# Kernel tuning notes

Hardware: AMD Instinct MI355X
Metric: run time of the kernel (lower is better)

Reference implementation:

```python
import jax, jax.numpy as jnp
import numpy as np
from jax import lax

DN = ('NCHW', 'OIHW', 'NCHW')  # torch conv layout
QMIN, QMAX = -128.0, 127.0     # qint8 range


def setup_inputs() -> dict:
    key = jax.random.key(0)
    k1, k2, k3, k4 = jax.random.split(key, 4)
    B, Cin, Cout, H, W, K = 8, 320, 320, 64, 64, 3
    x = jax.random.normal(k1, (B, Cin, H, W), dtype=jnp.float32)
    # int8 weight values stored as int32 (int_repr of per-channel quantized weight)
    weight_int = jax.random.randint(k2, (Cout, Cin, K, K), -128, 128, dtype=jnp.int32)
    weight_scales = jax.random.uniform(k3, (Cout,), jnp.float32, 0.001, 0.01)
    act_scales = jnp.float32(0.04)        # per-tensor activation scale
    act_zero_points = jnp.float32(3.0)    # per-tensor activation zero point
    act_scales_inv = 1.0 / act_scales
    bias = jax.random.normal(k4, (Cout,), dtype=jnp.float32) * 0.1
    # precomputed buffers (from_float): padding>0 path
    weight_sum_by_input_channels = weight_int.astype(jnp.float32).sum(axis=1, keepdims=True)  # [O,1,K,K]
    scale = weight_scales * act_scales  # fused dequant scale per output channel
    return {
        'x': x,
        'weight_int': weight_int,
        'weight_sum_by_input_channels': weight_sum_by_input_channels,
        'scale': scale,
        'act_scales_inv': act_scales_inv,
        'act_zero_points': act_zero_points,
        'bias': bias,
    }


def reference(x, weight_int, weight_sum_by_input_channels, scale,
              act_scales_inv, act_zero_points, bias):
    stride, pad = 1, 1
    # per-tensor activation quantization: x_int = clamp(round(x/s) + zp)
    x_int = jnp.clip(jnp.round(x * act_scales_inv) + act_zero_points, QMIN, QMAX)
    w = weight_int.astype(jnp.float32)
    # integer conv (emulated in f32): conv(x_int, W_int)
    acc = lax.conv_general_dilated(x_int, w, (stride, stride),
                                   [(pad, pad), (pad, pad)], dimension_numbers=DN)
    # zero-point correction: zp * conv(ones, sum_i W_int) (spatially varying near padding)
    ones = jnp.ones_like(x[:, :1])  # [B,1,H,W]
    corr = lax.conv_general_dilated(ones, weight_sum_by_input_channels, (stride, stride),
                                    [(pad, pad), (pad, pad)], dimension_numbers=DN)
    corr = corr * act_zero_points
    # dequant: per-output-channel scale = w_scale * a_scale, plus float bias
    out = scale[None, :, None, None] * (acc - corr) + bias[None, :, None, None]
    return out
```

## Files before the change

### kernel.cpp

```cpp
#include <hip/hip_runtime.h>
#include <hip/hip_bf16.h>


typedef int v4i __attribute__((ext_vector_type(4)));

typedef const unsigned int __attribute__((address_space(1)))* gas_uptr;
typedef unsigned int __attribute__((address_space(3)))* las_uptr;

#define B_   8
#define CIN  320
#define COUT 320
#define H_   64
#define W_   64
#define HW_  4096
#define HP   66
#define WP   66
#define XPAD_BYTES (B_*HP*WP*CIN)
#define W8_BYTES (COUT*9*CIN)

__global__ __launch_bounds__(256) void repack_bias_kernel(const int* __restrict__ wint,
                                                          unsigned char* __restrict__ w8,
                                                          const float* __restrict__ wsum,
                                                          const float* __restrict__ scale,
                                                          const float* __restrict__ bias,
                                                          const float* __restrict__ zp_p,
                                                          float* __restrict__ be) {
    int j = blockIdx.x * 256 + threadIdx.x;
    if (j < COUT) {
        float s = 0.f;
        #pragma unroll
        for (int tp = 0; tp < 9; ++tp) s += wsum[j*9 + tp];
        be[j] = bias[j] - scale[j] * zp_p[0] * s;
    }
    int co  = j / 720;
    int r   = j - co * 720;
    int tap = r / 80;
    int d   = r - tap * 80;
    int ci  = d * 4;
    const int* base = wint + (co * CIN + ci) * 9 + tap;
    unsigned b0 = (unsigned)(base[0]  & 0xFF);
    unsigned b1 = (unsigned)(base[9]  & 0xFF);
    unsigned b2 = (unsigned)(base[18] & 0xFF);
    unsigned b3 = (unsigned)(base[27] & 0xFF);
    ((unsigned*)w8)[j] = b0 | (b1 << 8) | (b2 << 16) | (b3 << 24);
}

__global__ __launch_bounds__(256) void quant_pad_kernel(const float* __restrict__ x,
                                                        unsigned char* __restrict__ xpad,
                                                        const float* __restrict__ inv_p,
                                                        const float* __restrict__ zp_p) {
    __shared__ __align__(16) unsigned lds[64 * 81];
    int bid = blockIdx.x;
    int b  = bid / HP;
    int ph = bid - b * HP;
    int t  = threadIdx.x;
    float inv = inv_p[0];
    float zp  = zp_p[0];
    int zpi = (int)rintf(zp);
    unsigned zd = ((unsigned)(zpi & 0xFF)) * 0x01010101u;

    unsigned* rowbase = (unsigned*)(xpad + (size_t)((b * HP + ph) * WP) * CIN);

    if (ph == 0 || ph == HP - 1) {
        for (int j = t; j < WP * CIN / 4; j += 256) rowbase[j] = zd;
        return;
    }
    int h = ph - 1;
    const float* xrow = x + (size_t)b * CIN * H_ * W_ + h * W_;
    int wq = t & 15;
    int cg = t >> 4;
    #pragma unroll
    for (int i = 0; i < 5; ++i) {
        int ci0 = i * 64 + cg * 4;
        float4 f[4];
        #pragma unroll
        for (int jj = 0; jj < 4; ++jj)
            f[jj] = *(const float4*)(xrow + (size_t)(ci0 + jj) * HW_ + wq * 4);
        #pragma unroll
        for (int k = 0; k < 4; ++k) {
            unsigned d = 0;
            #pragma unroll
            for (int jj = 0; jj < 4; ++jj) {
                float v = (&f[jj].x)[k];
                float q = rintf(v * inv) + zp;
                q = fminf(fmaxf(q, -128.0f), 127.0f);
                int qi = (int)q;
                d |= ((unsigned)(qi & 0xFF)) << (8 * jj);
            }
            lds[(wq * 4 + k) * 81 + (ci0 >> 2)] = d;
        }
    }
    __syncthreads();
    if (t < 80)            rowbase[t] = zd;
    else if (t < 160)      rowbase[65 * 80 + (t - 80)] = zd;
    for (int j = t; j < 64 * 80; j += 256) {
        int p = j / 80;
        int d = j - p * 80;
        rowbase[80 + j] = lds[p * 81 + d];
    }
}

#define CHUNK_SLOTS 1056
#define ROUNDS 5
#define BUF_BYTES (ROUNDS * 256 * 16)

__global__ __launch_bounds__(256, 2) void conv_gemm_kernel(const unsigned char* __restrict__ xpad,
                                                           const unsigned char* __restrict__ w8,
                                                           const float* __restrict__ scale,
                                                           const float* __restrict__ be,
                                                           float* __restrict__ out) {
    __shared__ __align__(16) unsigned char Al[2 * BUF_BYTES];

    int t    = threadIdx.x;
    int lane = t & 63;
    int wave = t >> 6;
    int wm   = wave & 1;
    int wn   = wave >> 1;
    int m0   = blockIdx.x * 128;
    int n0   = blockIdx.y * 160;
    int b0   = m0 >> 12;
    int h0   = (m0 & 4095) >> 6;

    int srcoff[ROUNDS];
    #pragma unroll
    for (int r = 0; r < ROUNDS; ++r) {
        int slot = r * 256 + t;
        if (slot >= CHUNK_SLOTS) slot = 0;
        int R   = slot / 264;
        int rem = slot - R * 264;
        int C   = rem >> 2;
        int ql  = rem & 3;
        int qs  = ql ^ (C & 3);
        srcoff[r] = ((b0 * HP + h0 + R) * WP + C) * CIN + qs * 16;
    }

    int colc = lane & 15;
    int q    = lane >> 4;

    int aoffs[3][4];
    #pragma unroll
    for (int kw = 0; kw < 3; ++kw)
        #pragma unroll
        for (int mi = 0; mi < 4; ++mi) {
            int C = mi * 16 + colc + kw;
            aoffs[kw][mi] = C * 64 + ((q ^ (C & 3)) * 16);
        }

    const unsigned char* bptr[5];
    #pragma unroll
    for (int ni = 0; ni < 5; ++ni) {
        int co = n0 + wn * 80 + ni * 16 + colc;
        bptr[ni] = w8 + (size_t)co * (9 * CIN) + q * 16;
    }

    v4i acc[4][5];
    v4i zero = {0, 0, 0, 0};
    #pragma unroll
    for (int mi = 0; mi < 4; ++mi)
        #pragma unroll
        for (int ni = 0; ni < 5; ++ni) acc[mi][ni] = zero;

    v4i bC[5], bN[5], aC[4], aN[4];
    #pragma unroll
    for (int ni = 0; ni < 5; ++ni)
        bC[ni] = *(const v4i*)(bptr[ni]);
    #pragma unroll
    for (int r = 0; r < ROUNDS; ++r)
        __builtin_amdgcn_global_load_lds((gas_uptr)(const void*)(xpad + srcoff[r]),
                                         (las_uptr)(Al + r * 4096 + t * 16), 16, 0, 0);
    __syncthreads();

    #pragma unroll 1
    for (int c = 0; c < 5; ++c) {
        if (c < 4) {
            unsigned char* dst = Al + ((c + 1) & 1) * BUF_BYTES;
            int ci = (c + 1) * 64;
            #pragma unroll
            for (int r = 0; r < ROUNDS; ++r)
                __builtin_amdgcn_global_load_lds((gas_uptr)(const void*)(xpad + srcoff[r] + ci),
                                                 (las_uptr)(dst + r * 4096 + t * 16), 16, 0, 0);
        }
        const unsigned char* ab = Al + (c & 1) * BUF_BYTES;
        int coff = c * 64;

        #pragma unroll
        for (int mi = 0; mi < 4; ++mi)
            aC[mi] = *(const v4i*)(ab + wm * 4224 + aoffs[0][mi]);

        #pragma unroll
        for (int tp = 0; tp < 9; ++tp) {
            int kh = tp / 3;
            if (tp < 8) {
                int tn  = tp + 1;
                int kh2 = tn / 3;
                int kw2 = tn - kh2 * 3;
                #pragma unroll
                for (int ni = 0; ni < 5; ++ni)
                    bN[ni] = *(const v4i*)(bptr[ni] + tn * CIN + coff);
                #pragma unroll
                for (int mi = 0; mi < 4; ++mi)
                    aN[mi] = *(const v4i*)(ab + (wm + kh2) * 4224 + aoffs[kw2][mi]);
            } else if (c < 4) {
                #pragma unroll
                for (int ni = 0; ni < 5; ++ni)
                    bN[ni] = *(const v4i*)(bptr[ni] + coff + 64);
            }
            #pragma unroll
            for (int mi = 0; mi < 4; ++mi)
                #pragma unroll
                for (int ni = 0; ni < 5; ++ni)
                    acc[mi][ni] = __builtin_amdgcn_mfma_i32_16x16x64_i8(aC[mi], bC[ni], acc[mi][ni], 0, 0, 0);
            if (tp < 8) {
                #pragma unroll
                for (int mi = 0; mi < 4; ++mi) aC[mi] = aN[mi];
            }
            if (tp < 8 || c < 4) {
                #pragma unroll
                for (int ni = 0; ni < 5; ++ni) bC[ni] = bN[ni];
            }
        }
        __syncthreads();
    }

    #pragma unroll
    for (int ni = 0; ni < 5; ++ni) {
        int co = n0 + wn * 80 + ni * 16 + colc;
        float s  = scale[co];
        float bz = be[co];
        #pragma unroll
        for (int mi = 0; mi < 4; ++mi) {
            int pix = m0 + wm * 64 + mi * 16 + q * 4;
            int bb2 = pix >> 12;
            int hw  = pix & 4095;
            v4i v = acc[mi][ni];
            float4 o;
            o.x = s * (float)v.x + bz;
            o.y = s * (float)v.y + bz;
            o.z = s * (float)v.z + bz;
            o.w = s * (float)v.w + bz;
            *(float4*)(out + (size_t)(bb2 * COUT + co) * HW_ + hw) = o;
        }
    }
}

extern "C" void kernel_launch(void* const* d_in, const int* in_sizes, int n_in,
                              void* d_out, int out_size, void* d_ws, size_t ws_size,
                              hipStream_t stream) {
    const float* x     = (const float*)d_in[0];
    const int*   wint  = (const int*)d_in[1];
    const float* wsum  = (const float*)d_in[2];
    const float* scale = (const float*)d_in[3];
    const float* inv_p = (const float*)d_in[4];
    const float* zp_p  = (const float*)d_in[5];
    const float* bias  = (const float*)d_in[6];
    float* out = (float*)d_out;

    unsigned char* xpad = (unsigned char*)d_ws;
    unsigned char* w8   = xpad + XPAD_BYTES;
    float*         be   = (float*)(w8 + W8_BYTES);

    repack_bias_kernel<<<(COUT * 720) / 256, 256, 0, stream>>>(wint, w8, wsum, scale, bias, zp_p, be);
    quant_pad_kernel<<<B_ * HP, 256, 0, stream>>>(x, xpad, inv_p, zp_p);

    dim3 grid((B_ * H_ * W_) / 128, COUT / 160);
    conv_gemm_kernel<<<grid, 256, 0, stream>>>(xpad, w8, scale, be, out);
}
```

Measured before the change: 149.4 us.

## Repack int8 weights into MFMA fragment order and change LDS swizzle

The weight repack kernel now writes int8 weights in the exact per-lane fragment order used by the MFMA loop, grouped by 16-channel output tile, tap and input chunk. Each wave's B loads then read contiguous 1KB blocks instead of strided rows. The activation LDS swizzle key also changes from C&3 to (C>>1)&3, meant to reduce bank conflicts on the shifted-column A reads. The weight buffer layout is now tied to this kernel's tiling.

```diff
diff --git a/kernel.cpp b/kernel.cpp
--- a/kernel.cpp
+++ b/kernel.cpp
@@ -42,7 +42,16 @@
     unsigned b1 = (unsigned)(base[9]  & 0xFF);
     unsigned b2 = (unsigned)(base[18] & 0xFF);
     unsigned b3 = (unsigned)(base[27] & 0xFF);
-    ((unsigned*)w8)[j] = b0 | (b1 << 8) | (b2 << 16) | (b3 << 24);
+    unsigned dword = b0 | (b1 << 8) | (b2 << 16) | (b3 << 24);
+
+    int coT   = co >> 4;
+    int colc  = co & 15;
+    int chunk = ci >> 6;
+    int q     = (ci >> 4) & 3;
+    int dw    = (ci >> 2) & 3;
+    int lane  = q * 16 + colc;
+    int idx   = (((coT * 9 + tap) * 5 + chunk) * 64 + lane) * 4 + dw;
+    ((unsigned*)w8)[idx] = dword;
 }
 
 __global__ __launch_bounds__(256) void quant_pad_kernel(const float* __restrict__ x,
@@ -130,7 +139,7 @@
         int rem = slot - R * 264;
         int C   = rem >> 2;
         int ql  = rem & 3;
-        int qs  = ql ^ (C & 3);
+        int qs  = ql ^ ((C >> 1) & 3);
         srcoff[r] = ((b0 * HP + h0 + R) * WP + C) * CIN + qs * 16;
     }
 
@@ -143,15 +152,14 @@
         #pragma unroll
         for (int mi = 0; mi < 4; ++mi) {
             int C = mi * 16 + colc + kw;
-            aoffs[kw][mi] = C * 64 + ((q ^ (C & 3)) * 16);
-        }
-
-    const unsigned char* bptr[5];
-    #pragma unroll
-    for (int ni = 0; ni < 5; ++ni) {
-        int co = n0 + wn * 80 + ni * 16 + colc;
-        bptr[ni] = w8 + (size_t)co * (9 * CIN) + q * 16;
-    }
+            aoffs[kw][mi] = C * 64 + ((q ^ ((C >> 1) & 3)) * 16);
+        }
+
+    const unsigned char* bbase[5];
+    int coT0 = (n0 >> 4) + wn * 5;
+    #pragma unroll
+    for (int ni = 0; ni < 5; ++ni)
+        bbase[ni] = w8 + (size_t)(coT0 + ni) * (45 * 1024) + lane * 16;
 
     v4i acc[4][5];
     v4i zero = {0, 0, 0, 0};
@@ -163,7 +171,7 @@
     v4i bC[5], bN[5], aC[4], aN[4];
     #pragma unroll
     for (int ni = 0; ni < 5; ++ni)
-        bC[ni] = *(const v4i*)(bptr[ni]);
+        bC[ni] = *(const v4i*)(bbase[ni]);
     #pragma unroll
     for (int r = 0; r < ROUNDS; ++r)
         __builtin_amdgcn_global_load_lds((gas_uptr)(const void*)(xpad + srcoff[r]),
@@ -181,7 +189,6 @@
                                                  (las_uptr)(dst + r * 4096 + t * 16), 16, 0, 0);
         }
         const unsigned char* ab = Al + (c & 1) * BUF_BYTES;
-        int coff = c * 64;
 
         #pragma unroll
         for (int mi = 0; mi < 4; ++mi)
@@ -189,21 +196,20 @@
 
         #pragma unroll
         for (int tp = 0; tp < 9; ++tp) {
-            int kh = tp / 3;
             if (tp < 8) {
                 int tn  = tp + 1;
                 int kh2 = tn / 3;
                 int kw2 = tn - kh2 * 3;
                 #pragma unroll
                 for (int ni = 0; ni < 5; ++ni)
-                    bN[ni] = *(const v4i*)(bptr[ni] + tn * CIN + coff);
+                    bN[ni] = *(const v4i*)(bbase[ni] + (tn * 5 + c) * 1024);
                 #pragma unroll
                 for (int mi = 0; mi < 4; ++mi)
                     aN[mi] = *(const v4i*)(ab + (wm + kh2) * 4224 + aoffs[kw2][mi]);
             } else if (c < 4) {
                 #pragma unroll
                 for (int ni = 0; ni < 5; ++ni)
-                    bN[ni] = *(const v4i*)(bptr[ni] + coff + 64);
+                    bN[ni] = *(const v4i*)(bbase[ni] + (c + 1) * 1024);
             }
             #pragma unroll
             for (int mi = 0; mi < 4; ++mi)
```

New measurement: 141.0 us. 5.7% less time.
